# Kernel tuning notes

Measured on AMD Instinct MI355X. Metric: run time of the kernel, lower is better.

Reference implementation:

```python
import jax, jax.numpy as jnp
import numpy as np

B, S, DIN = 4, 2048, 1024
H, D = 16, 64  # num_head, per-head dim_out


def _xavier(key, shape):
    fan_in, fan_out = shape[0], shape[1]
    limit = float(np.sqrt(6.0 / (fan_in + fan_out)))
    return jax.random.uniform(key, shape, jnp.float32, -limit, limit)


def setup_inputs() -> dict:
    key = jax.random.key(0)
    k_x, k_q, k_k, k_v, k_o = jax.random.split(key, 5)
    inputs = jax.random.normal(k_x, (B, S, DIN), jnp.float32)
    # weights stored as [in, out] (transpose of torch Linear.weight); bias zeros
    return {
        "inputs": inputs,
        "wq": _xavier(k_q, (DIN, H * D)), "bq": jnp.zeros((H * D,), jnp.float32),
        "wk": _xavier(k_k, (DIN, H * D)), "bk": jnp.zeros((H * D,), jnp.float32),
        "wv": _xavier(k_v, (DIN, H * D)), "bv": jnp.zeros((H * D,), jnp.float32),
        "wo": _xavier(k_o, (H * D, D)),  "bo": jnp.zeros((D,), jnp.float32),
    }


def reference(inputs, wq, bq, wk, bk, wv, bv, wo, bo):
    b, s, _ = inputs.shape
    q = (inputs @ wq + bq).reshape(b, s, H, D).transpose(0, 2, 1, 3)  # bhsd
    k = (inputs @ wk + bk).reshape(b, s, H, D).transpose(0, 2, 1, 3)
    v = (inputs @ wv + bv).reshape(b, s, H, D).transpose(0, 2, 1, 3)
    scores = jnp.einsum('bhsd,bhSd->bhsS', q, k) / jnp.sqrt(jnp.float32(D))
    p = jax.nn.softmax(scores, axis=-1)
    o = jnp.einsum('bhsS,bhSd->bhsd', p, v)
    o = o.transpose(0, 2, 1, 3).reshape(b, s, H * D)
    return o @ wo + bo  # [b, s, D]
```

## Files before the change

### kernel.cpp

```cpp
#include <hip/hip_runtime.h>

typedef __attribute__((ext_vector_type(8))) __bf16 bf16x8;
typedef __attribute__((ext_vector_type(4))) float f32x4;

#define NB   4
#define NS   2048
#define NDIN 1024
#define NH   16
#define ND   64
#define NHD  1024
#define NM   (NB * NS)

__device__ __forceinline__ float bf2f(unsigned short u) {
    unsigned int x = ((unsigned int)u) << 16;
    return __builtin_bit_cast(float, x);
}
__device__ __forceinline__ unsigned short f2bf(float f) {
    unsigned int u = __builtin_bit_cast(unsigned int, f);
    u += 0x7fff + ((u >> 16) & 1);
    return (unsigned short)(u >> 16);
}
__device__ __forceinline__ unsigned int cvt_pk_bf16(float lo, float hi) {
    unsigned int r;
    asm("v_cvt_pk_bf16_f32 %0, %1, %2" : "=v"(r) : "v"(lo), "v"(hi));
    return r;
}
__device__ __forceinline__ void gload16(const unsigned short* g, unsigned short* l) {
    __builtin_amdgcn_global_load_lds((const __attribute__((address_space(1))) unsigned int*)g,
                                     (__attribute__((address_space(3))) unsigned int*)l, 16, 0, 0);
}

__global__ __launch_bounds__(256) void cvt_x(const float* __restrict__ src,
                                             unsigned short* __restrict__ dst) {
    int i = blockIdx.x * 256 + threadIdx.x;
    float4 a = ((const float4*)src)[i * 2];
    float4 b = ((const float4*)src)[i * 2 + 1];
    union { uint4 u; unsigned short s[8]; } o;
    o.s[0] = f2bf(a.x); o.s[1] = f2bf(a.y); o.s[2] = f2bf(a.z); o.s[3] = f2bf(a.w);
    o.s[4] = f2bf(b.x); o.s[5] = f2bf(b.y); o.s[6] = f2bf(b.z); o.s[7] = f2bf(b.w);
    *(uint4*)(dst + (size_t)i * 8) = o.u;
}

__global__ void transpose_cvt(const float* __restrict__ src,
                              unsigned short* __restrict__ dst, int K, int N) {
    __shared__ unsigned short t[32][33];
    int k0 = blockIdx.x * 32, n0 = blockIdx.y * 32;
    int tx = threadIdx.x, ty = threadIdx.y;
#pragma unroll
    for (int i = 0; i < 32; i += 8)
        t[ty + i][tx] = f2bf(src[(size_t)(k0 + ty + i) * N + (n0 + tx)]);
    __syncthreads();
#pragma unroll
    for (int i = 0; i < 32; i += 8)
        dst[(size_t)(n0 + ty + i) * K + (k0 + tx)] = t[tx][ty + i];
}

__global__ __launch_bounds__(256) void gemm_qkv(
    const unsigned short* __restrict__ X, const unsigned short* __restrict__ Wt,
    const float* __restrict__ bq, const float* __restrict__ bk,
    const float* __restrict__ bv,
    unsigned short* __restrict__ Q, unsigned short* __restrict__ K,
    unsigned short* __restrict__ V) {
    __shared__ unsigned short Al[128][32];
    __shared__ unsigned short Bl[128][32];
    int mb = blockIdx.x * 128;
    int nb = blockIdx.y * 128;
    int tid = threadIdx.x;
    int wid = tid >> 6, lane = tid & 63, quad = lane >> 4, l16 = lane & 15;
    int wm = (wid & 1) * 64, wn = (wid >> 1) * 64;

    int srow = 16 * wid + (lane >> 2);
    int scol = (lane & 3) * 8;
    const unsigned short* pa0 = X + (size_t)(mb + srow) * NDIN + scol;
    const unsigned short* pa1 = pa0 + (size_t)64 * NDIN;
    const unsigned short* pb0 = Wt + (size_t)(nb + srow) * NDIN + scol;
    const unsigned short* pb1 = pb0 + (size_t)64 * NDIN;
    unsigned short* la = &Al[0][0] + wid * 512;
    unsigned short* lb = &Bl[0][0] + wid * 512;

    f32x4 acc[4][4];
#pragma unroll
    for (int i = 0; i < 4; i++)
#pragma unroll
        for (int j = 0; j < 4; j++) acc[i][j] = (f32x4){0.f, 0.f, 0.f, 0.f};

    for (int k0 = 0; k0 < NDIN; k0 += 32) {
        gload16(pa0, la);
        gload16(pa1, la + 2048);
        gload16(pb0, lb);
        gload16(pb1, lb + 2048);
        pa0 += 32; pa1 += 32; pb0 += 32; pb1 += 32;
        __syncthreads();
        bf16x8 af[4], bfr[4];
#pragma unroll
        for (int i = 0; i < 4; i++)
            af[i] = *(const bf16x8*)(&Al[wm + i * 16 + l16][quad * 8]);
#pragma unroll
        for (int j = 0; j < 4; j++)
            bfr[j] = *(const bf16x8*)(&Bl[wn + j * 16 + l16][quad * 8]);
#pragma unroll
        for (int i = 0; i < 4; i++)
#pragma unroll
            for (int j = 0; j < 4; j++)
                acc[i][j] = __builtin_amdgcn_mfma_f32_16x16x32_bf16(af[i], bfr[j], acc[i][j], 0, 0, 0);
        __syncthreads();
    }

#pragma unroll
    for (int i = 0; i < 4; i++) {
#pragma unroll
        for (int j = 0; j < 4; j++) {
            int n = nb + wn + j * 16 + l16;
            int wsel = n >> 10;
            int cc = n & 1023;
            const float* bias = (wsel == 0) ? bq : (wsel == 1) ? bk : bv;
            unsigned short* dstp = (wsel == 0) ? Q : (wsel == 1) ? K : V;
            float bias_v = bias[cc];
            int h = cc >> 6, d = cc & 63;
#pragma unroll
            for (int r = 0; r < 4; r++) {
                int m = mb + wm + i * 16 + quad * 4 + r;
                int b = m >> 11, s = m & 2047;
                dstp[((size_t)((b * NH + h) * NS + s)) * ND + d] = f2bf(acc[i][j][r] + bias_v);
            }
        }
    }
}

__global__ __launch_bounds__(256) void attn(
    const unsigned short* __restrict__ Q, const unsigned short* __restrict__ K,
    const unsigned short* __restrict__ V, unsigned short* __restrict__ Obuf) {
    __shared__ unsigned short Kl[2][64][64];
    __shared__ unsigned short Vt[2][64][64];

    int lin = blockIdx.x;
    int xcd = lin & 7, idx = lin >> 3;
    int bh = ((idx >> 4) << 3) | xcd;
    int qt = idx & 15;

    size_t base = (size_t)bh * NS * ND;
    int tid = threadIdx.x, wid = tid >> 6, lane = tid & 63;
    int quad = lane >> 4, l16 = lane & 15;
    int lx = l16 & 7;
    int q0 = qt * 128 + wid * 32;

    bf16x8 qa[2][2];
#pragma unroll
    for (int s = 0; s < 2; s++)
#pragma unroll
        for (int f = 0; f < 2; f++) {
            union { uint4 u; unsigned short sv[8]; } in_, out_;
            in_.u = *(const uint4*)(Q + base + (size_t)(q0 + s * 16 + l16) * ND + f * 32 + quad * 8);
#pragma unroll
            for (int j = 0; j < 8; j++) out_.sv[j] = f2bf(bf2f(in_.sv[j]) * 0.125f);
            qa[s][f] = __builtin_bit_cast(bf16x8, out_.u);
        }

    float lrow[2] = {0.f, 0.f};
    f32x4 o[2][4];
#pragma unroll
    for (int s = 0; s < 2; s++)
#pragma unroll
        for (int t = 0; t < 4; t++) o[s][t] = (f32x4){0.f, 0.f, 0.f, 0.f};

    int c0 = tid, c1 = tid + 256;
    int kr0w = c0 >> 3, kc0 = c0 & 7, kg0c = kc0 ^ (kr0w & 7);
    int kr1w = c1 >> 3, kc1 = c1 & 7, kg1c = kc1 ^ (kr1w & 7);
    const unsigned short* kp0 = K + base + (size_t)kr0w * ND + kc0 * 8;
    const unsigned short* kp1 = K + base + (size_t)kr1w * ND + kc1 * 8;
    int p = tid & 31, dqA = tid >> 5, dqB = dqA + 8;
    int cp = ((p >> 4) << 2) | ((p >> 1) & 3);
    int ps = (((p >> 3) & 1) << 2) | ((p & 1) << 1);
    int cb = cp ^ ((dqA & 1) << 2);
    const unsigned short* vg = V + base + (size_t)(2 * p) * ND + dqA * 4;

    uint4 k0r, k1r;
    uint2 va0, va1, va2, va3;

    auto writeKV = [&](int buf) {
        *(uint4*)(&Kl[buf][kr0w][kg0c * 8]) = k0r;
        *(uint4*)(&Kl[buf][kr1w][kg1c * 8]) = k1r;
        unsigned short* vt = &Vt[buf][0][0];
        unsigned int w0 = __builtin_amdgcn_perm(va1.x, va0.x, 0x05040100u);
        unsigned int w1 = __builtin_amdgcn_perm(va1.x, va0.x, 0x07060302u);
        unsigned int w2 = __builtin_amdgcn_perm(va1.y, va0.y, 0x05040100u);
        unsigned int w3 = __builtin_amdgcn_perm(va1.y, va0.y, 0x07060302u);
        *(unsigned int*)(vt + (dqA * 4 + 0) * 64 + ((cb ^ 0) << 3) + ps) = w0;
        *(unsigned int*)(vt + (dqA * 4 + 1) * 64 + ((cb ^ 1) << 3) + ps) = w1;
        *(unsigned int*)(vt + (dqA * 4 + 2) * 64 + ((cb ^ 2) << 3) + ps) = w2;
        *(unsigned int*)(vt + (dqA * 4 + 3) * 64 + ((cb ^ 3) << 3) + ps) = w3;
        unsigned int x0 = __builtin_amdgcn_perm(va3.x, va2.x, 0x05040100u);
        unsigned int x1 = __builtin_amdgcn_perm(va3.x, va2.x, 0x07060302u);
        unsigned int x2 = __builtin_amdgcn_perm(va3.y, va2.y, 0x05040100u);
        unsigned int x3 = __builtin_amdgcn_perm(va3.y, va2.y, 0x07060302u);
        *(unsigned int*)(vt + (dqB * 4 + 0) * 64 + ((cb ^ 0) << 3) + ps) = x0;
        *(unsigned int*)(vt + (dqB * 4 + 1) * 64 + ((cb ^ 1) << 3) + ps) = x1;
        *(unsigned int*)(vt + (dqB * 4 + 2) * 64 + ((cb ^ 2) << 3) + ps) = x2;
        *(unsigned int*)(vt + (dqB * 4 + 3) * 64 + ((cb ^ 3) << 3) + ps) = x3;
    };

    k0r = *(const uint4*)kp0;
    k1r = *(const uint4*)kp1;
    va0 = *(const uint2*)(vg);
    va1 = *(const uint2*)(vg + ND);
    va2 = *(const uint2*)(vg + 32);
    va3 = *(const uint2*)(vg + ND + 32);
    writeKV(0);
    __syncthreads();

    int cur = 0;
    for (int kc = 0; kc < NS; kc += 64) {
        bool more = (kc + 64 < NS);
        if (more) {
            kp0 += 64 * ND; kp1 += 64 * ND; vg += 64 * ND;
            k0r = *(const uint4*)kp0;
            k1r = *(const uint4*)kp1;
            va0 = *(const uint2*)(vg);
            va1 = *(const uint2*)(vg + ND);
            va2 = *(const uint2*)(vg + 32);
            va3 = *(const uint2*)(vg + ND + 32);
        }

        const unsigned short (*Kc)[64] = Kl[cur];
        const unsigned short (*Vc)[64] = Vt[cur];

        f32x4 st[2][4];
#pragma unroll
        for (int sub = 0; sub < 4; sub++) {
            bf16x8 kb0 = *(const bf16x8*)(&Kc[sub * 16 + l16][((quad ^ lx) << 3)]);
            bf16x8 kb1 = *(const bf16x8*)(&Kc[sub * 16 + l16][(((4 + quad) ^ lx) << 3)]);
#pragma unroll
            for (int s = 0; s < 2; s++) {
                f32x4 c = (f32x4){0.f, 0.f, 0.f, 0.f};
                c = __builtin_amdgcn_mfma_f32_16x16x32_bf16(kb0, qa[s][0], c, 0, 0, 0);
                c = __builtin_amdgcn_mfma_f32_16x16x32_bf16(kb1, qa[s][1], c, 0, 0, 0);
                st[s][sub] = c;
            }
        }

        bf16x8 pb[2][2];
#pragma unroll
        for (int s = 0; s < 2; s++) {
            float sum = 0.f;
#pragma unroll
            for (int sub = 0; sub < 4; sub++)
#pragma unroll
                for (int r = 0; r < 4; r++) {
                    float pv = __expf(st[s][sub][r]);
                    st[s][sub][r] = pv;
                    sum += pv;
                }
            sum += __shfl_xor(sum, 16, 64);
            sum += __shfl_xor(sum, 32, 64);
            lrow[s] += sum;
            unsigned int a0 = cvt_pk_bf16(st[s][0][0], st[s][0][1]);
            unsigned int a1 = cvt_pk_bf16(st[s][0][2], st[s][0][3]);
            unsigned int a2 = cvt_pk_bf16(st[s][1][0], st[s][1][1]);
            unsigned int a3 = cvt_pk_bf16(st[s][1][2], st[s][1][3]);
            pb[s][0] = __builtin_bit_cast(bf16x8, (uint4){a0, a1, a2, a3});
            unsigned int b0 = cvt_pk_bf16(st[s][2][0], st[s][2][1]);
            unsigned int b1 = cvt_pk_bf16(st[s][2][2], st[s][2][3]);
            unsigned int b2 = cvt_pk_bf16(st[s][3][0], st[s][3][1]);
            unsigned int b3 = cvt_pk_bf16(st[s][3][2], st[s][3][3]);
            pb[s][1] = __builtin_bit_cast(bf16x8, (uint4){b0, b1, b2, b3});
        }

#pragma unroll
        for (int t = 0; t < 4; t++) {
            bf16x8 vb0 = *(const bf16x8*)(&Vc[t * 16 + l16][((quad ^ lx) << 3)]);
            bf16x8 vb1 = *(const bf16x8*)(&Vc[t * 16 + l16][(((4 + quad) ^ lx) << 3)]);
#pragma unroll
            for (int s = 0; s < 2; s++) {
                o[s][t] = __builtin_amdgcn_mfma_f32_16x16x32_bf16(vb0, pb[s][0], o[s][t], 0, 0, 0);
                o[s][t] = __builtin_amdgcn_mfma_f32_16x16x32_bf16(vb1, pb[s][1], o[s][t], 0, 0, 0);
            }
        }

        if (more) {
            int nxt = cur ^ 1;
            writeKV(nxt);
            __syncthreads();
            cur = nxt;
        }
    }

    int b = bh >> 4, h = bh & 15;
#pragma unroll
    for (int s = 0; s < 2; s++) {
        float inv = 1.0f / lrow[s];
        int q = q0 + s * 16 + l16;
#pragma unroll
        for (int t = 0; t < 4; t++) {
            uint2 w;
            w.x = cvt_pk_bf16(o[s][t][0] * inv, o[s][t][1] * inv);
            w.y = cvt_pk_bf16(o[s][t][2] * inv, o[s][t][3] * inv);
            *(uint2*)(Obuf + (size_t)(b * NS + q) * NHD + h * ND + t * 16 + quad * 4) = w;
        }
    }
}

__global__ __launch_bounds__(64) void out_proj(
    const unsigned short* __restrict__ Obuf, const unsigned short* __restrict__ WoT,
    const float* __restrict__ bo, float* __restrict__ Out) {
    int m0 = blockIdx.x * 16;
    int lane = threadIdx.x, quad = lane >> 4, l16 = lane & 15;
    f32x4 acc[4];
#pragma unroll
    for (int t = 0; t < 4; t++) acc[t] = (f32x4){0.f, 0.f, 0.f, 0.f};
    for (int k0 = 0; k0 < NHD; k0 += 32) {
        bf16x8 a = *(const bf16x8*)(Obuf + (size_t)(m0 + l16) * NHD + k0 + quad * 8);
#pragma unroll
        for (int t = 0; t < 4; t++) {
            bf16x8 b = *(const bf16x8*)(WoT + (size_t)(t * 16 + l16) * NHD + k0 + quad * 8);
            acc[t] = __builtin_amdgcn_mfma_f32_16x16x32_bf16(a, b, acc[t], 0, 0, 0);
        }
    }
#pragma unroll
    for (int t = 0; t < 4; t++) {
        int n = t * 16 + l16;
        float bb = bo[n];
#pragma unroll
        for (int r = 0; r < 4; r++) {
            int m = m0 + quad * 4 + r;
            Out[(size_t)m * ND + n] = acc[t][r] + bb;
        }
    }
}

extern "C" void kernel_launch(void* const* d_in, const int* in_sizes, int n_in,
                              void* d_out, int out_size, void* d_ws, size_t ws_size,
                              hipStream_t stream) {
    const float* X  = (const float*)d_in[0];
    const float* wq = (const float*)d_in[1];
    const float* bq = (const float*)d_in[2];
    const float* wk = (const float*)d_in[3];
    const float* bk = (const float*)d_in[4];
    const float* wv = (const float*)d_in[5];
    const float* bv = (const float*)d_in[6];
    const float* wo = (const float*)d_in[7];
    const float* bo = (const float*)d_in[8];
    float* Out = (float*)d_out;

    char* w = (char*)d_ws;
    unsigned short* Wt  = (unsigned short*)w; w += (size_t)3072 * 1024 * 2;
    unsigned short* WoT = (unsigned short*)w; w += (size_t)64 * 1024 * 2;
    unsigned short* Xb  = (unsigned short*)w; w += (size_t)NM * NDIN * 2;
    unsigned short* Qb  = (unsigned short*)w; w += (size_t)NM * NHD * 2;
    unsigned short* Kb  = (unsigned short*)w; w += (size_t)NM * NHD * 2;
    unsigned short* Vb  = (unsigned short*)w; w += (size_t)NM * NHD * 2;
    unsigned short* Ob  = (unsigned short*)w; w += (size_t)NM * NHD * 2;

    cvt_x<<<NM * NDIN / (256 * 8), 256, 0, stream>>>(X, Xb);

    dim3 tb(32, 8);
    transpose_cvt<<<dim3(32, 32), tb, 0, stream>>>(wq, Wt, 1024, 1024);
    transpose_cvt<<<dim3(32, 32), tb, 0, stream>>>(wk, Wt + 1024 * 1024, 1024, 1024);
    transpose_cvt<<<dim3(32, 32), tb, 0, stream>>>(wv, Wt + 2 * 1024 * 1024, 1024, 1024);
    transpose_cvt<<<dim3(32, 2),  tb, 0, stream>>>(wo, WoT, 1024, 64);

    gemm_qkv<<<dim3(64, 24), 256, 0, stream>>>(Xb, Wt, bq, bk, bv, Qb, Kb, Vb);
    attn<<<1024, 256, 0, stream>>>(Qb, Kb, Vb, Ob);
    out_proj<<<512, 64, 0, stream>>>(Ob, WoT, bo, Out);
}
```

Measured before the change: 270.7 us.

## Stage QKV epilogue through LDS, merge weight transposes, tune attention scheduling

The QKV GEMM epilogue now writes bf16 results into a swizzled LDS tile and then issues 16-byte coalesced row stores, replacing scattered 2-byte global stores. The three weight transposes are merged into one launch. In attention, MFMA phases get raised wave priority, V fragment loads are hoisted ahead of the softmax, and the per-row sum shuffle reduction is deferred to the end. The extra 32KB LDS in the GEMM may reduce occupancy, and the attention changes raise register pressure.

```diff
diff --git a/kernel.cpp b/kernel.cpp
--- a/kernel.cpp
+++ b/kernel.cpp
@@ -41,6 +41,22 @@
     *(uint4*)(dst + (size_t)i * 8) = o.u;
 }
 
+__global__ void transpose_cvt3(const float* __restrict__ wq, const float* __restrict__ wk,
+                               const float* __restrict__ wv, unsigned short* __restrict__ dst_all) {
+    __shared__ unsigned short t[32][33];
+    const float* src = blockIdx.z == 0 ? wq : blockIdx.z == 1 ? wk : wv;
+    unsigned short* dst = dst_all + (size_t)blockIdx.z * 1024 * 1024;
+    int k0 = blockIdx.x * 32, n0 = blockIdx.y * 32;
+    int tx = threadIdx.x, ty = threadIdx.y;
+#pragma unroll
+    for (int i = 0; i < 32; i += 8)
+        t[ty + i][tx] = f2bf(src[(size_t)(k0 + ty + i) * 1024 + (n0 + tx)]);
+    __syncthreads();
+#pragma unroll
+    for (int i = 0; i < 32; i += 8)
+        dst[(size_t)(n0 + ty + i) * 1024 + (k0 + tx)] = t[tx][ty + i];
+}
+
 __global__ void transpose_cvt(const float* __restrict__ src,
                               unsigned short* __restrict__ dst, int K, int N) {
     __shared__ unsigned short t[32][33];
@@ -63,6 +79,7 @@
     unsigned short* __restrict__ V) {
     __shared__ unsigned short Al[128][32];
     __shared__ unsigned short Bl[128][32];
+    __shared__ unsigned short Cl[128][128];
     int mb = blockIdx.x * 128;
     int nb = blockIdx.y * 128;
     int tid = threadIdx.x;
@@ -106,23 +123,32 @@
         __syncthreads();
     }
 
-#pragma unroll
-    for (int i = 0; i < 4; i++) {
+    int wsel = nb >> 10;
+    const float* bias = (wsel == 0) ? bq : (wsel == 1) ? bk : bv;
+    unsigned short* dstp = (wsel == 0) ? Q : (wsel == 1) ? K : V;
+#pragma unroll
+    for (int i = 0; i < 4; i++)
 #pragma unroll
         for (int j = 0; j < 4; j++) {
-            int n = nb + wn + j * 16 + l16;
-            int wsel = n >> 10;
-            int cc = n & 1023;
-            const float* bias = (wsel == 0) ? bq : (wsel == 1) ? bk : bv;
-            unsigned short* dstp = (wsel == 0) ? Q : (wsel == 1) ? K : V;
-            float bias_v = bias[cc];
-            int h = cc >> 6, d = cc & 63;
+            int nl = wn + j * 16 + l16;
+            float bias_v = bias[(nb & 1023) + nl];
 #pragma unroll
             for (int r = 0; r < 4; r++) {
-                int m = mb + wm + i * 16 + quad * 4 + r;
-                int b = m >> 11, s = m & 2047;
-                dstp[((size_t)((b * NH + h) * NS + s)) * ND + d] = f2bf(acc[i][j][r] + bias_v);
+                int ml = wm + i * 16 + quad * 4 + r;
+                int pc = ((nl >> 3) ^ (ml & 15));
+                Cl[ml][(pc << 3) | (nl & 7)] = f2bf(acc[i][j][r] + bias_v);
             }
+        }
+    __syncthreads();
+    {
+        int hl = tid >> 7, sl = tid & 127;
+        int h = ((nb & 1023) >> 6) + hl;
+        int m = mb + sl, b = m >> 11, sidx = m & 2047;
+        unsigned short* orow = dstp + ((size_t)((b * NH + h) * NS + sidx)) * ND;
+#pragma unroll
+        for (int c = 0; c < 8; c++) {
+            int pc = ((hl * 8 + c) ^ (sl & 15));
+            *(uint4*)(orow + c * 8) = *(const uint4*)(&Cl[sl][pc << 3]);
         }
     }
 }
@@ -225,6 +251,7 @@
         const unsigned short (*Vc)[64] = Vt[cur];
 
         f32x4 st[2][4];
+        __builtin_amdgcn_s_setprio(1);
 #pragma unroll
         for (int sub = 0; sub < 4; sub++) {
             bf16x8 kb0 = *(const bf16x8*)(&Kc[sub * 16 + l16][((quad ^ lx) << 3)]);
@@ -237,6 +264,14 @@
                 st[s][sub] = c;
             }
         }
+        __builtin_amdgcn_s_setprio(0);
+
+        bf16x8 vb[4][2];
+#pragma unroll
+        for (int t = 0; t < 4; t++) {
+            vb[t][0] = *(const bf16x8*)(&Vc[t * 16 + l16][((quad ^ lx) << 3)]);
+            vb[t][1] = *(const bf16x8*)(&Vc[t * 16 + l16][(((4 + quad) ^ lx) << 3)]);
+        }
 
         bf16x8 pb[2][2];
 #pragma unroll
@@ -250,8 +285,6 @@
                     st[s][sub][r] = pv;
                     sum += pv;
                 }
-            sum += __shfl_xor(sum, 16, 64);
-            sum += __shfl_xor(sum, 32, 64);
             lrow[s] += sum;
             unsigned int a0 = cvt_pk_bf16(st[s][0][0], st[s][0][1]);
             unsigned int a1 = cvt_pk_bf16(st[s][0][2], st[s][0][3]);
@@ -265,16 +298,15 @@
             pb[s][1] = __builtin_bit_cast(bf16x8, (uint4){b0, b1, b2, b3});
         }
 
-#pragma unroll
-        for (int t = 0; t < 4; t++) {
-            bf16x8 vb0 = *(const bf16x8*)(&Vc[t * 16 + l16][((quad ^ lx) << 3)]);
-            bf16x8 vb1 = *(const bf16x8*)(&Vc[t * 16 + l16][(((4 + quad) ^ lx) << 3)]);
+        __builtin_amdgcn_s_setprio(1);
+#pragma unroll
+        for (int t = 0; t < 4; t++)
 #pragma unroll
             for (int s = 0; s < 2; s++) {
-                o[s][t] = __builtin_amdgcn_mfma_f32_16x16x32_bf16(vb0, pb[s][0], o[s][t], 0, 0, 0);
-                o[s][t] = __builtin_amdgcn_mfma_f32_16x16x32_bf16(vb1, pb[s][1], o[s][t], 0, 0, 0);
+                o[s][t] = __builtin_amdgcn_mfma_f32_16x16x32_bf16(vb[t][0], pb[s][0], o[s][t], 0, 0, 0);
+                o[s][t] = __builtin_amdgcn_mfma_f32_16x16x32_bf16(vb[t][1], pb[s][1], o[s][t], 0, 0, 0);
             }
-        }
+        __builtin_amdgcn_s_setprio(0);
 
         if (more) {
             int nxt = cur ^ 1;
@@ -287,7 +319,10 @@
     int b = bh >> 4, h = bh & 15;
 #pragma unroll
     for (int s = 0; s < 2; s++) {
-        float inv = 1.0f / lrow[s];
+        float ls = lrow[s];
+        ls += __shfl_xor(ls, 16, 64);
+        ls += __shfl_xor(ls, 32, 64);
+        float inv = 1.0f / ls;
         int q = q0 + s * 16 + l16;
 #pragma unroll
         for (int t = 0; t < 4; t++) {
@@ -353,10 +388,8 @@
     cvt_x<<<NM * NDIN / (256 * 8), 256, 0, stream>>>(X, Xb);
 
     dim3 tb(32, 8);
-    transpose_cvt<<<dim3(32, 32), tb, 0, stream>>>(wq, Wt, 1024, 1024);
-    transpose_cvt<<<dim3(32, 32), tb, 0, stream>>>(wk, Wt + 1024 * 1024, 1024, 1024);
-    transpose_cvt<<<dim3(32, 32), tb, 0, stream>>>(wv, Wt + 2 * 1024 * 1024, 1024, 1024);
-    transpose_cvt<<<dim3(32, 2),  tb, 0, stream>>>(wo, WoT, 1024, 64);
+    transpose_cvt3<<<dim3(32, 32, 3), tb, 0, stream>>>(wq, wk, wv, Wt);
+    transpose_cvt<<<dim3(32, 2), tb, 0, stream>>>(wo, WoT, 1024, 64);
 
     gemm_qkv<<<dim3(64, 24), 256, 0, stream>>>(Xb, Wt, bq, bk, bv, Qb, Kb, Vb);
     attn<<<1024, 256, 0, stream>>>(Qb, Kb, Vb, Ob);
```

Measured after the change: 269.9 us. Within noise of the previous version (-0.3%).
